# Optimization experiments

Hardware: AMD Instinct MI355X
Metric: run time of the kernel (lower is better)

Reference implementation:

```python
import jax, jax.numpy as jnp
import numpy as np

N_NODES = 100000
N_EDGES = 1600000
K = 4
D = 16  # d_in // K
NEG_SLOPE = 0.01  # F.leaky_relu default
EPS = 1e-12       # F.normalize default eps


def setup_inputs() -> dict:
    key = jax.random.key(0)
    k1, k2, k3 = jax.random.split(key, 3)
    f_in = jax.random.normal(k1, (N_NODES, K, D), dtype=jnp.float32)
    edges = jax.random.randint(k2, (N_EDGES, 2), 0, N_NODES, dtype=jnp.int64)
    attn_w = jax.random.normal(k3, (K, 2 * D), dtype=jnp.float32) * 0.1
    return {"f_in": f_in, "edges": edges, "attn_w": attn_w}


def reference(f_in, edges, attn_w):
    # f_in: [N, K, D], edges: [E, 2] (src, dst), attn_w: [K, 2D]
    src = edges[:, 0]
    dst = edges[:, 1]
    f_src = f_in[src]            # [E, K, D] gather
    f_dst = f_in[dst]            # [E, K, D] gather
    f_edge = jnp.concatenate([f_src, f_dst], axis=2)  # [E, K, 2D]
    # per-factor attention score + leaky_relu
    score = jnp.einsum('ekd,kd->ek', f_edge, attn_w)  # [E, K]
    score = jnp.where(score >= 0, score, NEG_SLOPE * score)
    # scatter_softmax over edges grouped by src, per factor
    smax = jax.ops.segment_max(score, src, num_segments=N_NODES)  # [N, K]
    smax = jnp.where(jnp.isfinite(smax), smax, 0.0)  # empty segments -> -inf -> 0
    ex = jnp.exp(score - smax[src])                               # [E, K]
    denom = jax.ops.segment_sum(ex, src, num_segments=N_NODES)    # [N, K]
    norm = ex / denom[src]                                        # [E, K]
    # weighted scatter_add of neighbor embeddings
    m = jax.ops.segment_sum(f_dst * norm[:, :, None], src, num_segments=N_NODES)  # [N, K, D]
    # F.normalize(m): L2 over dim=1 (factor axis)
    l2 = jnp.sqrt(jnp.sum(m * m, axis=1, keepdims=True))  # [N, 1, D]
    return m / jnp.maximum(l2, EPS)
```

## Files before the change

### kernel.cpp

```cpp
#include <hip/hip_runtime.h>

#define N_NODES 100000
#define N_EDGES 1600000
#define KH 4
#define DH 16
#define KD (KH * DH)
#define MAXDEG 64
#define NEG_SLOPE 0.01f

#define T 256
#define NPART 8
#define PART_SZ ((N_NODES + NPART - 1) / NPART)
#define SCORE_BLOCKS 1568
#define SCATTER_PB 256
#define SCATTER_BLOCKS (SCATTER_PB * NPART)
#define AGG_BLOCKS ((PART_SZ / 4) * NPART)

__device__ __forceinline__ float lrelu(float x) {
    return (x >= 0.f) ? x : NEG_SLOPE * x;
}

__global__ void k_pre(const float* __restrict__ f_in,
                      const float* __restrict__ attn_w,
                      const int* __restrict__ edges,
                      float* __restrict__ a_src,
                      float* __restrict__ a_dst,
                      int* __restrict__ deg,
                      int* __restrict__ dst_pad) {
    if (blockIdx.x < SCORE_BLOCKS) {
        int i = blockIdx.x * T + threadIdx.x;
        if (i >= N_NODES * KH) return;
        int k = i & (KH - 1);
        const float4* f  = (const float4*)(f_in + (size_t)i * DH);
        const float4* w1 = (const float4*)(attn_w + k * 2 * DH);
        const float4* w2 = (const float4*)(attn_w + k * 2 * DH + DH);
        float s1 = 0.f, s2 = 0.f;
#pragma unroll
        for (int j = 0; j < DH / 4; ++j) {
            float4 fv = f[j];
            float4 av = w1[j];
            float4 bv = w2[j];
            s1 += fv.x * av.x + fv.y * av.y + fv.z * av.z + fv.w * av.w;
            s2 += fv.x * bv.x + fv.y * bv.y + fv.z * bv.z + fv.w * bv.w;
        }
        a_src[i] = s1;
        a_dst[i] = s2;
    } else {
        int sb = blockIdx.x - SCORE_BLOCKS;
        int p  = sb & (NPART - 1);
        int q  = sb >> 3;
        int lo = p * PART_SZ;
        int hi = lo + PART_SZ;
        const long long* e2 = (const long long*)edges;
        const int npair = N_EDGES / 2;
        for (int i = q * T + threadIdx.x; i < npair; i += SCATTER_PB * T) {
            long long v0 = __builtin_nontemporal_load(&e2[2 * i]);
            long long v1 = __builtin_nontemporal_load(&e2[2 * i + 1]);
            int s0 = (int)(v0 & 0xffffffffLL);
            int d0 = (int)(v0 >> 32);
            int s1 = (int)(v1 & 0xffffffffLL);
            int d1 = (int)(v1 >> 32);
            if (s0 >= lo && s0 < hi) {
                int pos = atomicAdd(&deg[s0], 1);
                if (pos < MAXDEG)
                    dst_pad[(size_t)s0 * MAXDEG + pos] = d0;
            }
            if (s1 >= lo && s1 < hi) {
                int pos = atomicAdd(&deg[s1], 1);
                if (pos < MAXDEG)
                    dst_pad[(size_t)s1 * MAXDEG + pos] = d1;
            }
        }
    }
}

__global__ void k_node_aggregate(const int* __restrict__ deg,
                                 const int* __restrict__ dst_pad,
                                 const float* __restrict__ a_src,
                                 const float* __restrict__ a_dst,
                                 const float* __restrict__ f_in,
                                 float* __restrict__ out) {
    int p    = blockIdx.x & (NPART - 1);
    int q    = blockIdx.x >> 3;
    int wid  = threadIdx.x >> 6;
    int lane = threadIdx.x & 63;
    int n    = p * PART_SZ + q * 4 + wid;
    if (n >= N_NODES) return;
    int g  = lane >> 4;
    int m  = lane & 15;
    int kk = m >> 2;

    int dg = deg[n];
    if (dg > MAXDEG) dg = MAXDEG;
    float as = a_src[n * KH + kk];
    const int* dl = dst_pad + (size_t)n * MAXDEG;

    float4 acc = make_float4(0.f, 0.f, 0.f, 0.f);
    float dsum = 0.f;
    int i = 0;
    int dg8 = dg & ~7;
    for (; i < dg8; i += 8) {
        int dA = dl[i + g];
        int dB = dl[i + 4 + g];
        float4 fA = *(const float4*)(f_in + (size_t)dA * KD + 4 * m);
        float4 fB = *(const float4*)(f_in + (size_t)dB * KD + 4 * m);
        float aA = a_dst[dA * KH + kk];
        float aB = a_dst[dB * KH + kk];
        float eA = __expf(lrelu(as + aA));
        float eB = __expf(lrelu(as + aB));
        dsum += eA + eB;
        acc.x += eA * fA.x + eB * fB.x;
        acc.y += eA * fA.y + eB * fB.y;
        acc.z += eA * fA.z + eB * fB.z;
        acc.w += eA * fA.w + eB * fB.w;
    }
    for (; i < dg; i += 4) {
        if (i + g < dg) {
            int d = dl[i + g];
            float4 fv = *(const float4*)(f_in + (size_t)d * KD + 4 * m);
            float e = __expf(lrelu(as + a_dst[d * KH + kk]));
            dsum += e;
            acc.x += e * fv.x;
            acc.y += e * fv.y;
            acc.z += e * fv.z;
            acc.w += e * fv.w;
        }
    }

    dsum  += __shfl_xor(dsum, 16);  dsum  += __shfl_xor(dsum, 32);
    acc.x += __shfl_xor(acc.x, 16); acc.x += __shfl_xor(acc.x, 32);
    acc.y += __shfl_xor(acc.y, 16); acc.y += __shfl_xor(acc.y, 32);
    acc.z += __shfl_xor(acc.z, 16); acc.z += __shfl_xor(acc.z, 32);
    acc.w += __shfl_xor(acc.w, 16); acc.w += __shfl_xor(acc.w, 32);

    float invd = (dsum > 0.f) ? (1.f / dsum) : 0.f;
    float4 v = make_float4(acc.x * invd, acc.y * invd, acc.z * invd, acc.w * invd);

    float sx = v.x * v.x, sy = v.y * v.y, sz = v.z * v.z, sw = v.w * v.w;
    sx += __shfl_xor(sx, 4); sx += __shfl_xor(sx, 8);
    sy += __shfl_xor(sy, 4); sy += __shfl_xor(sy, 8);
    sz += __shfl_xor(sz, 4); sz += __shfl_xor(sz, 8);
    sw += __shfl_xor(sw, 4); sw += __shfl_xor(sw, 8);
    float ix = 1.f / fmaxf(sqrtf(sx), 1e-12f);
    float iy = 1.f / fmaxf(sqrtf(sy), 1e-12f);
    float iz = 1.f / fmaxf(sqrtf(sz), 1e-12f);
    float iw = 1.f / fmaxf(sqrtf(sw), 1e-12f);

    if (g == 0) {
        float4 o = make_float4(v.x * ix, v.y * iy, v.z * iz, v.w * iw);
        *(float4*)(out + (size_t)n * KD + 4 * m) = o;
    }
}

extern "C" void kernel_launch(void* const* d_in, const int* in_sizes, int n_in,
                              void* d_out, int out_size, void* d_ws, size_t ws_size,
                              hipStream_t stream) {
    const float* f_in   = (const float*)d_in[0];
    const int*   edges  = (const int*)d_in[1];
    const float* attn_w = (const float*)d_in[2];
    float* out = (float*)d_out;

    float* a_src  = (float*)d_ws;
    float* a_dst  = a_src + N_NODES * KH;
    int*   deg    = (int*)(a_dst + N_NODES * KH);
    int*   dst_pad= deg + N_NODES;

    (void)hipMemsetAsync(deg, 0, (size_t)N_NODES * sizeof(int), stream);

    k_pre<<<SCORE_BLOCKS + SCATTER_BLOCKS, T, 0, stream>>>(f_in, attn_w, edges,
                                                           a_src, a_dst, deg, dst_pad);
    k_node_aggregate<<<AGG_BLOCKS, T, 0, stream>>>(deg, dst_pad, a_src, a_dst, f_in, out);
}
```

Baseline: 228.6 us.

## Gather neighbor features from fp16 copy and split fused pre-kernel

The score kernel now also writes an fp16 copy of the node features, and the aggregation kernel gathers neighbor rows from that half-size copy when workspace allows. This halves the bytes of the random gathers that dominate aggregation. The fused pre-kernel is split into separate score and scatter launches, which adds a launch and loses the overlap between the two phases. It also adds an extra write pass and fp16 rounding error in the weighted sum.

New measurement: 222.2 us. -2.8%, faster.

```diff
diff --git a/kernel.cpp b/kernel.cpp
--- a/kernel.cpp
+++ b/kernel.cpp
@@ -1,4 +1,5 @@
 #include <hip/hip_runtime.h>
+#include <hip/hip_fp16.h>
 
 #define N_NODES 100000
 #define N_EDGES 1600000
@@ -11,7 +12,7 @@
 #define T 256
 #define NPART 8
 #define PART_SZ ((N_NODES + NPART - 1) / NPART)
-#define SCORE_BLOCKS 1568
+#define SCORE_GRID ((N_NODES * KH + T - 1) / T)
 #define SCATTER_PB 256
 #define SCATTER_BLOCKS (SCATTER_PB * NPART)
 #define AGG_BLOCKS ((PART_SZ / 4) * NPART)
@@ -20,65 +21,74 @@
     return (x >= 0.f) ? x : NEG_SLOPE * x;
 }
 
-__global__ void k_pre(const float* __restrict__ f_in,
-                      const float* __restrict__ attn_w,
-                      const int* __restrict__ edges,
-                      float* __restrict__ a_src,
-                      float* __restrict__ a_dst,
-                      int* __restrict__ deg,
-                      int* __restrict__ dst_pad) {
-    if (blockIdx.x < SCORE_BLOCKS) {
-        int i = blockIdx.x * T + threadIdx.x;
-        if (i >= N_NODES * KH) return;
-        int k = i & (KH - 1);
-        const float4* f  = (const float4*)(f_in + (size_t)i * DH);
-        const float4* w1 = (const float4*)(attn_w + k * 2 * DH);
-        const float4* w2 = (const float4*)(attn_w + k * 2 * DH + DH);
-        float s1 = 0.f, s2 = 0.f;
+__global__ void k_scores(const float* __restrict__ f_in,
+                         const float* __restrict__ attn_w,
+                         float* __restrict__ a_src,
+                         float* __restrict__ a_dst,
+                         __half* __restrict__ f16) {
+    int i = blockIdx.x * T + threadIdx.x;
+    if (i >= N_NODES * KH) return;
+    int k = i & (KH - 1);
+    const float4* f  = (const float4*)(f_in + (size_t)i * DH);
+    const float4* w1 = (const float4*)(attn_w + k * 2 * DH);
+    const float4* w2 = (const float4*)(attn_w + k * 2 * DH + DH);
+    float s1 = 0.f, s2 = 0.f;
+    __half2 h[8];
 #pragma unroll
-        for (int j = 0; j < DH / 4; ++j) {
-            float4 fv = f[j];
-            float4 av = w1[j];
-            float4 bv = w2[j];
-            s1 += fv.x * av.x + fv.y * av.y + fv.z * av.z + fv.w * av.w;
-            s2 += fv.x * bv.x + fv.y * bv.y + fv.z * bv.z + fv.w * bv.w;
-        }
-        a_src[i] = s1;
-        a_dst[i] = s2;
-    } else {
-        int sb = blockIdx.x - SCORE_BLOCKS;
-        int p  = sb & (NPART - 1);
-        int q  = sb >> 3;
-        int lo = p * PART_SZ;
-        int hi = lo + PART_SZ;
-        const long long* e2 = (const long long*)edges;
-        const int npair = N_EDGES / 2;
-        for (int i = q * T + threadIdx.x; i < npair; i += SCATTER_PB * T) {
-            long long v0 = __builtin_nontemporal_load(&e2[2 * i]);
-            long long v1 = __builtin_nontemporal_load(&e2[2 * i + 1]);
-            int s0 = (int)(v0 & 0xffffffffLL);
-            int d0 = (int)(v0 >> 32);
-            int s1 = (int)(v1 & 0xffffffffLL);
-            int d1 = (int)(v1 >> 32);
-            if (s0 >= lo && s0 < hi) {
-                int pos = atomicAdd(&deg[s0], 1);
-                if (pos < MAXDEG)
-                    dst_pad[(size_t)s0 * MAXDEG + pos] = d0;
-            }
-            if (s1 >= lo && s1 < hi) {
-                int pos = atomicAdd(&deg[s1], 1);
-                if (pos < MAXDEG)
-                    dst_pad[(size_t)s1 * MAXDEG + pos] = d1;
-            }
-        }
-    }
-}
-
+    for (int j = 0; j < DH / 4; ++j) {
+        float4 fv = f[j];
+        float4 av = w1[j];
+        float4 bv = w2[j];
+        s1 += fv.x * av.x + fv.y * av.y + fv.z * av.z + fv.w * av.w;
+        s2 += fv.x * bv.x + fv.y * bv.y + fv.z * bv.z + fv.w * bv.w;
+        h[2 * j]     = __floats2half2_rn(fv.x, fv.y);
+        h[2 * j + 1] = __floats2half2_rn(fv.z, fv.w);
+    }
+    a_src[i] = s1;
+    a_dst[i] = s2;
+    if (f16) {
+        uint4* dst = (uint4*)(f16 + (size_t)i * DH);
+        dst[0] = *(const uint4*)&h[0];
+        dst[1] = *(const uint4*)&h[4];
+    }
+}
+
+__global__ void k_scatter(const int* __restrict__ edges,
+                          int* __restrict__ deg,
+                          int* __restrict__ dst_pad) {
+    int p  = blockIdx.x & (NPART - 1);
+    int q  = blockIdx.x >> 3;
+    int lo = p * PART_SZ;
+    int hi = lo + PART_SZ;
+    const long long* e2 = (const long long*)edges;
+    const int npair = N_EDGES / 2;
+    for (int i = q * T + threadIdx.x; i < npair; i += SCATTER_PB * T) {
+        long long v0 = __builtin_nontemporal_load(&e2[2 * i]);
+        long long v1 = __builtin_nontemporal_load(&e2[2 * i + 1]);
+        int s0 = (int)(v0 & 0xffffffffLL);
+        int d0 = (int)(v0 >> 32);
+        int s1 = (int)(v1 & 0xffffffffLL);
+        int d1 = (int)(v1 >> 32);
+        if (s0 >= lo && s0 < hi) {
+            int pos = atomicAdd(&deg[s0], 1);
+            if (pos < MAXDEG)
+                dst_pad[(size_t)s0 * MAXDEG + pos] = d0;
+        }
+        if (s1 >= lo && s1 < hi) {
+            int pos = atomicAdd(&deg[s1], 1);
+            if (pos < MAXDEG)
+                dst_pad[(size_t)s1 * MAXDEG + pos] = d1;
+        }
+    }
+}
+
+template <bool USE_F16>
 __global__ void k_node_aggregate(const int* __restrict__ deg,
                                  const int* __restrict__ dst_pad,
                                  const float* __restrict__ a_src,
                                  const float* __restrict__ a_dst,
                                  const float* __restrict__ f_in,
+                                 const __half* __restrict__ f16,
                                  float* __restrict__ out) {
     int p    = blockIdx.x & (NPART - 1);
     int q    = blockIdx.x >> 3;
@@ -102,10 +112,25 @@
     for (; i < dg8; i += 8) {
         int dA = dl[i + g];
         int dB = dl[i + 4 + g];
-        float4 fA = *(const float4*)(f_in + (size_t)dA * KD + 4 * m);
-        float4 fB = *(const float4*)(f_in + (size_t)dB * KD + 4 * m);
-        float aA = a_dst[dA * KH + kk];
-        float aB = a_dst[dB * KH + kk];
+        float4 fA, fB;
+        float aA, aB;
+        if constexpr (USE_F16) {
+            uint2 hA = *(const uint2*)(f16 + (size_t)dA * KD + 4 * m);
+            uint2 hB = *(const uint2*)(f16 + (size_t)dB * KD + 4 * m);
+            aA = a_dst[dA * KH + kk];
+            aB = a_dst[dB * KH + kk];
+            float2 A01 = __half22float2(*(const __half2*)&hA.x);
+            float2 A23 = __half22float2(*(const __half2*)&hA.y);
+            float2 B01 = __half22float2(*(const __half2*)&hB.x);
+            float2 B23 = __half22float2(*(const __half2*)&hB.y);
+            fA = make_float4(A01.x, A01.y, A23.x, A23.y);
+            fB = make_float4(B01.x, B01.y, B23.x, B23.y);
+        } else {
+            fA = *(const float4*)(f_in + (size_t)dA * KD + 4 * m);
+            fB = *(const float4*)(f_in + (size_t)dB * KD + 4 * m);
+            aA = a_dst[dA * KH + kk];
+            aB = a_dst[dB * KH + kk];
+        }
         float eA = __expf(lrelu(as + aA));
         float eB = __expf(lrelu(as + aB));
         dsum += eA + eB;
@@ -117,7 +142,15 @@
     for (; i < dg; i += 4) {
         if (i + g < dg) {
             int d = dl[i + g];
-            float4 fv = *(const float4*)(f_in + (size_t)d * KD + 4 * m);
+            float4 fv;
+            if constexpr (USE_F16) {
+                uint2 hv = *(const uint2*)(f16 + (size_t)d * KD + 4 * m);
+                float2 v01 = __half22float2(*(const __half2*)&hv.x);
+                float2 v23 = __half22float2(*(const __half2*)&hv.y);
+                fv = make_float4(v01.x, v01.y, v23.x, v23.y);
+            } else {
+                fv = *(const float4*)(f_in + (size_t)d * KD + 4 * m);
+            }
             float e = __expf(lrelu(as + a_dst[d * KH + kk]));
             dsum += e;
             acc.x += e * fv.x;
@@ -160,14 +193,27 @@
     const float* attn_w = (const float*)d_in[2];
     float* out = (float*)d_out;
 
-    float* a_src  = (float*)d_ws;
-    float* a_dst  = a_src + N_NODES * KH;
-    int*   deg    = (int*)(a_dst + N_NODES * KH);
-    int*   dst_pad= deg + N_NODES;
+    float* a_src   = (float*)d_ws;
+    float* a_dst   = a_src + N_NODES * KH;
+    int*   deg     = (int*)(a_dst + N_NODES * KH);
+    int*   dst_pad = deg + N_NODES;
+    __half* f16    = (__half*)(dst_pad + (size_t)N_NODES * MAXDEG);
+
+    size_t need = (size_t)(2 * N_NODES * KH + N_NODES) * 4
+                + (size_t)N_NODES * MAXDEG * 4
+                + (size_t)N_NODES * KD * 2;
+    bool use16 = (ws_size >= need);
 
     (void)hipMemsetAsync(deg, 0, (size_t)N_NODES * sizeof(int), stream);
 
-    k_pre<<<SCORE_BLOCKS + SCATTER_BLOCKS, T, 0, stream>>>(f_in, attn_w, edges,
-                                                           a_src, a_dst, deg, dst_pad);
-    k_node_aggregate<<<AGG_BLOCKS, T, 0, stream>>>(deg, dst_pad, a_src, a_dst, f_in, out);
-}
+    k_scores<<<SCORE_GRID, T, 0, stream>>>(f_in, attn_w, a_src, a_dst,
+                                           use16 ? f16 : (__half*)nullptr);
+    k_scatter<<<SCATTER_BLOCKS, T, 0, stream>>>(edges, deg, dst_pad);
+    if (use16) {
+        k_node_aggregate<true><<<AGG_BLOCKS, T, 0, stream>>>(deg, dst_pad, a_src, a_dst,
+                                                             f_in, f16, out);
+    } else {
+        k_node_aggregate<false><<<AGG_BLOCKS, T, 0, stream>>>(deg, dst_pad, a_src, a_dst,
+                                                              f_in, f16, out);
+    }
+}
```
